# Kernel optimization log

Hardware: AMD Instinct MI355X
Metric: run time of the kernel (lower is better)

The kernel has to match this reference:

```python
import jax, jax.numpy as jnp
import numpy as np

QMIN, QMAX = -128, 127  # int8 range

def setup_inputs() -> dict:
    key = jax.random.key(0)
    k1, k2, k3 = jax.random.split(key, 3)
    B, S, DIN, DOUT = 8, 2048, 4096, 4096
    x = jax.random.normal(k1, (B, S, DIN), dtype=jnp.float32)
    weight = jax.random.normal(k2, (DOUT, DIN), dtype=jnp.float32) * 0.02
    bias = jax.random.normal(k3, (DOUT,), dtype=jnp.float32) * 0.01
    # per-tensor asymmetric activation qparams (as produced by a calibrated observer)
    act_scale = jnp.float32(0.05)
    act_zero_point = jnp.int32(3)
    # per-output-channel symmetric weight scales (block_size = (1, in_features))
    weight_scale = jnp.max(jnp.abs(weight), axis=1) / 127.0  # [DOUT]
    return {"x": x, "weight": weight, "bias": bias,
            "act_scale": act_scale, "act_zero_point": act_zero_point,
            "weight_scale": weight_scale}

def reference(x, weight, bias, act_scale, act_zero_point, weight_scale):
    # 1) quantize activations: per-tensor asymmetric int8
    qx = jnp.clip(jnp.round(x / act_scale) + act_zero_point, QMIN, QMAX).astype(jnp.int8)
    # 2) quantize weight: per-output-channel symmetric int8 (zero_point = 0)
    qw = jnp.clip(jnp.round(weight / weight_scale[:, None]), QMIN, QMAX).astype(jnp.int8)
    acc = jnp.einsum('bsk,nk->bsn',
                     qx.astype(jnp.int32) - act_zero_point.astype(jnp.int32),
                     qw.astype(jnp.int32))  # [B, S, DOUT] int32
    # 4) dequantize: combined scale = act_scale * weight_scale[n], then bias
    out = acc.astype(jnp.float32) * (act_scale * weight_scale) + bias
    return out
```

## Files before the change

### kernel.cpp

```cpp
#include <hip/hip_runtime.h>
#include <cstdint>

#define M_DIM 16384
#define N_DIM 4096
#define K_DIM 4096

#define BM 256
#define BN 256
#define BK 128

typedef __attribute__((ext_vector_type(4))) int int32x4;
typedef __attribute__((ext_vector_type(4))) float f32x4;

#define GLLD16(g, l)                                              \
  __builtin_amdgcn_global_load_lds(                               \
      (const __attribute__((address_space(1))) void*)(g),         \
      (__attribute__((address_space(3))) void*)(l), 16, 0, 0)

__global__ void quant_fused(const float* __restrict__ x,
                            const float* __restrict__ w,
                            const float* __restrict__ wscale,
                            const float* __restrict__ bias,
                            const float* __restrict__ sp,
                            const int* __restrict__ zpp,
                            int8_t* __restrict__ qx,
                            int8_t* __restrict__ qw,
                            float* __restrict__ cs,
                            float* __restrict__ off) {
  __shared__ int red[4];
  if (blockIdx.x < 16384) {
    const float rs = 1.0f / sp[0];
    const int zp = zpp[0];
    const size_t b = (size_t)blockIdx.x * 1024;
    const f32x4* x4 = (const f32x4*)x;
    unsigned* q4 = (unsigned*)qx;
#pragma unroll
    for (int i = 0; i < 4; i++) {
      const size_t idx = b + (size_t)i * 256 + threadIdx.x;
      f32x4 v = __builtin_nontemporal_load(&x4[idx]);
      int q0 = min(127, max(-128, (int)rintf(v[0] * rs) + zp));
      int q1 = min(127, max(-128, (int)rintf(v[1] * rs) + zp));
      int q2 = min(127, max(-128, (int)rintf(v[2] * rs) + zp));
      int q3 = min(127, max(-128, (int)rintf(v[3] * rs) + zp));
      q4[idx] = (unsigned)(q0 & 255) | ((unsigned)(q1 & 255) << 8) |
                ((unsigned)(q2 & 255) << 16) | ((unsigned)(q3 & 255) << 24);
    }
  } else {
    const int n = blockIdx.x - 16384;
    const float ws = wscale[n];
    const float rws = 1.0f / ws;
    const float s = sp[0];
    const int zp = zpp[0];
    const f32x4* wr = (const f32x4*)(w + (size_t)n * K_DIM);
    unsigned* qr = (unsigned*)(qw + (size_t)n * K_DIM);
    int sum = 0;
#pragma unroll
    for (int it = 0; it < K_DIM / (256 * 4); it++) {
      const int idx = it * 256 + threadIdx.x;
      f32x4 v = __builtin_nontemporal_load(&wr[idx]);
      int q0 = min(127, max(-128, (int)rintf(v[0] * rws)));
      int q1 = min(127, max(-128, (int)rintf(v[1] * rws)));
      int q2 = min(127, max(-128, (int)rintf(v[2] * rws)));
      int q3 = min(127, max(-128, (int)rintf(v[3] * rws)));
      sum += q0 + q1 + q2 + q3;
      qr[idx] = (unsigned)(q0 & 255) | ((unsigned)(q1 & 255) << 8) |
                ((unsigned)(q2 & 255) << 16) | ((unsigned)(q3 & 255) << 24);
    }
#pragma unroll
    for (int o = 32; o > 0; o >>= 1) sum += __shfl_down(sum, o, 64);
    if ((threadIdx.x & 63) == 0) red[threadIdx.x >> 6] = sum;
    __syncthreads();
    if (threadIdx.x == 0) {
      const int tot = red[0] + red[1] + red[2] + red[3];
      const float c = s * ws;
      cs[n] = c;
      off[n] = bias[n] - (float)(zp * tot) * c;
    }
  }
}

__global__ __launch_bounds__(512, 2) void gemm_i8(
    const int8_t* __restrict__ qx, const int8_t* __restrict__ qw,
    const float* __restrict__ cs, const float* __restrict__ off,
    float* __restrict__ out) {
  __shared__ __align__(16) int8_t lds[131072];

  const int tid = threadIdx.x;
  const int lane = tid & 63;
  const int wave = tid >> 6;
  const int wm = wave >> 2;
  const int wn = wave & 3;

  const int bid = blockIdx.x;
  const int swz = (bid & 7) * 128 + (bid >> 3);
  const int n0 = (swz & 15) * BN;
  const int m0 = (swz >> 4) * BM;

  int32x4 acc[8][4] = {};
  int32x4 af[8], bf0[4], bf1[4];

  const int scol = ((lane & 7) ^ ((lane >> 3) & 7)) * 16;
  const int8_t* pA[2][2];
  const int8_t* pB[2][2];
#pragma unroll
  for (int h = 0; h < 2; h++)
#pragma unroll
    for (int j = 0; j < 2; j++) {
      const int r = h * 128 + (wave * 2 + j) * 8 + (lane >> 3);
      const int ga = ((r >> 6) & 1) * 128 + (r >> 7) * 64 + (r & 63);
      const int gb = ((r >> 5) & 3) * 64 + (r >> 7) * 32 + (r & 31);
      pA[h][j] = qx + (size_t)(m0 + ga) * K_DIM + scol;
      pB[h][j] = qw + (size_t)(n0 + gb) * K_DIM + scol;
    }

  const int fr = lane & 15;
  const int quad = lane >> 4;
  int aoffs[8], boffs[4];
#pragma unroll
  for (int mtl = 0; mtl < 4; mtl++)
#pragma unroll
    for (int ks = 0; ks < 2; ks++) {
      const int r = wm * 64 + mtl * 16 + fr;
      const int c = (ks * 4 + quad) ^ (fr & 7);
      aoffs[mtl * 2 + ks] = r * 128 + c * 16;
    }
#pragma unroll
  for (int ntl = 0; ntl < 2; ntl++)
#pragma unroll
    for (int ks = 0; ks < 2; ks++) {
      const int r = wn * 32 + ntl * 16 + fr;
      const int c = (ks * 4 + quad) ^ (fr & 7);
      boffs[ntl * 2 + ks] = r * 128 + c * 16;
    }

#define STAGE(rbase, h, P, kb)                                          \
  do {                                                                  \
    GLLD16(P[h][0] + (kb), lds + (rbase) + (h) * 16384 + wave * 2048);  \
    GLLD16(P[h][1] + (kb),                                              \
           lds + (rbase) + (h) * 16384 + wave * 2048 + 1024);           \
  } while (0)

#define LDA(buf, h)                                                     \
  do {                                                                  \
    _Pragma("unroll") for (int q = 0; q < 8; q++) af[q] =               \
        *(const int32x4*)(lds + (buf) * 65536 + (h) * 16384 + aoffs[q]); \
  } while (0)

#define LDB(buf, g, BF)                                                 \
  do {                                                                  \
    _Pragma("unroll") for (int q = 0; q < 4; q++) BF[q] =               \
        *(const int32x4*)(lds + (buf) * 65536 + 32768 + (g) * 16384 +   \
                          boffs[q]);                                    \
  } while (0)

#define MM(h, g, BF)                                                       \
  do {                                                                    \
    _Pragma("unroll") for (int mtl = 0; mtl < 4; mtl++)                   \
        _Pragma("unroll") for (int ntl = 0; ntl < 2; ntl++) {             \
      acc[(h)*4 + mtl][(g)*2 + ntl] = __builtin_amdgcn_mfma_i32_16x16x64_i8( \
          BF[ntl * 2 + 0], af[mtl * 2 + 0], acc[(h)*4 + mtl][(g)*2 + ntl], \
          0, 0, 0);                                                        \
      acc[(h)*4 + mtl][(g)*2 + ntl] = __builtin_amdgcn_mfma_i32_16x16x64_i8( \
          BF[ntl * 2 + 1], af[mtl * 2 + 1], acc[(h)*4 + mtl][(g)*2 + ntl], \
          0, 0, 0);                                                        \
    }                                                                      \
  } while (0)

#define BAR() __builtin_amdgcn_s_barrier()
#define WAITLGKM() asm volatile("s_waitcnt lgkmcnt(0)" ::: "memory")
#define VM8() asm volatile("s_waitcnt vmcnt(8)" ::: "memory")
#define PRIO(x) __builtin_amdgcn_s_setprio(x)

  STAGE(0, 0, pA, 0);
  STAGE(0, 1, pA, 0);
  STAGE(32768, 0, pB, 0);
  STAGE(32768, 1, pB, 0);
  STAGE(65536, 0, pA, 128);
  STAGE(65536, 1, pA, 128);
  STAGE(98304, 0, pB, 128);
  STAGE(98304, 1, pB, 128);
  VM8();
  BAR();

  for (int i = 0; i < K_DIM / (2 * BK); i++) {
    const int kb1 = ((2 * i + 1) << 7) & (K_DIM - 1);
    const int kb2 = ((2 * i + 2) << 7) & (K_DIM - 1);
    const int kb3 = ((2 * i + 3) << 7) & (K_DIM - 1);
    LDA(0, 0);
    LDB(0, 0, bf0);
    LDB(0, 1, bf1);
    WAITLGKM();
    PRIO(1); MM(0, 0, bf0); PRIO(0);
    STAGE(65536, 1, pA, kb1);
    PRIO(1); MM(0, 1, bf1); PRIO(0);
    VM8();
    BAR();
    LDA(0, 1);
    WAITLGKM();
    PRIO(1); MM(1, 1, bf1); PRIO(0);
    STAGE(0, 0, pA, kb2);
    STAGE(32768, 0, pB, kb2);
    STAGE(32768, 1, pB, kb2);
    PRIO(1); MM(1, 0, bf0); PRIO(0);
    VM8();
    BAR();
    LDA(1, 0);
    LDB(1, 0, bf0);
    LDB(1, 1, bf1);
    WAITLGKM();
    PRIO(1); MM(0, 0, bf0); PRIO(0);
    STAGE(0, 1, pA, kb2);
    PRIO(1); MM(0, 1, bf1); PRIO(0);
    VM8();
    BAR();
    LDA(1, 1);
    WAITLGKM();
    PRIO(1); MM(1, 1, bf1); PRIO(0);
    STAGE(65536, 0, pA, kb3);
    STAGE(98304, 0, pB, kb3);
    STAGE(98304, 1, pB, kb3);
    PRIO(1); MM(1, 0, bf0); PRIO(0);
    VM8();
    BAR();
  }

#pragma unroll
  for (int nt = 0; nt < 4; nt++) {
    const int colb = n0 + wn * 64 + nt * 16 + quad * 4;
    const f32x4 c4 = *(const f32x4*)(cs + colb);
    const f32x4 o4 = *(const f32x4*)(off + colb);
#pragma unroll
    for (int mt = 0; mt < 8; mt++) {
      const int row = m0 + wm * 128 + mt * 16 + fr;
      f32x4 v;
      v[0] = (float)acc[mt][nt][0] * c4[0] + o4[0];
      v[1] = (float)acc[mt][nt][1] * c4[1] + o4[1];
      v[2] = (float)acc[mt][nt][2] * c4[2] + o4[2];
      v[3] = (float)acc[mt][nt][3] * c4[3] + o4[3];
      __builtin_nontemporal_store(
          v, (f32x4*)(out + (size_t)row * N_DIM + colb));
    }
  }
#undef STAGE
#undef LDA
#undef LDB
#undef MM
#undef BAR
#undef WAITLGKM
#undef VM8
#undef PRIO
}

extern "C" void kernel_launch(void* const* d_in, const int* in_sizes, int n_in,
                              void* d_out, int out_size, void* d_ws,
                              size_t ws_size, hipStream_t stream) {
  const float* x = (const float*)d_in[0];
  const float* w = (const float*)d_in[1];
  const float* bias = (const float*)d_in[2];
  const float* act_scale = (const float*)d_in[3];
  const int* zp = (const int*)d_in[4];
  const float* wscale = (const float*)d_in[5];
  float* out = (float*)d_out;

  int8_t* qx = (int8_t*)d_ws;
  int8_t* qw = qx + (size_t)M_DIM * K_DIM;
  float* cs = (float*)(qw + (size_t)N_DIM * K_DIM);
  float* off = cs + N_DIM;

  quant_fused<<<16384 + N_DIM, 256, 0, stream>>>(x, w, wscale, bias,
                                                 act_scale, zp, qx, qw, cs,
                                                 off);
  gemm_i8<<<dim3((M_DIM / BM) * (N_DIM / BN)), 512, 0, stream>>>(qx, qw, cs,
                                                                 off, out);
}
```

Measured before the change: 661.3 us.

## Double-buffer A fragments and prefetch LDS reads ahead of MFMA blocks

```diff
diff --git a/kernel.cpp b/kernel.cpp
--- a/kernel.cpp
+++ b/kernel.cpp
@@ -97,7 +97,7 @@
   const int m0 = (swz >> 4) * BM;
 
   int32x4 acc[8][4] = {};
-  int32x4 af[8], bf0[4], bf1[4];
+  int32x4 afA[8], afB[8], bf0[4], bf1[4];
 
   const int scol = ((lane & 7) ^ ((lane >> 3) & 7)) * 16;
   const int8_t* pA[2][2];
@@ -140,9 +140,9 @@
            lds + (rbase) + (h) * 16384 + wave * 2048 + 1024);           \
   } while (0)
 
-#define LDA(buf, h)                                                     \
+#define LDA(buf, h, AF)                                                 \
   do {                                                                  \
-    _Pragma("unroll") for (int q = 0; q < 8; q++) af[q] =               \
+    _Pragma("unroll") for (int q = 0; q < 8; q++) AF[q] =               \
         *(const int32x4*)(lds + (buf) * 65536 + (h) * 16384 + aoffs[q]); \
   } while (0)
 
@@ -153,22 +153,23 @@
                           boffs[q]);                                    \
   } while (0)
 
-#define MM(h, g, BF)                                                       \
+#define MM(h, g, BF, AF)                                                   \
   do {                                                                    \
     _Pragma("unroll") for (int mtl = 0; mtl < 4; mtl++)                   \
         _Pragma("unroll") for (int ntl = 0; ntl < 2; ntl++) {             \
       acc[(h)*4 + mtl][(g)*2 + ntl] = __builtin_amdgcn_mfma_i32_16x16x64_i8( \
-          BF[ntl * 2 + 0], af[mtl * 2 + 0], acc[(h)*4 + mtl][(g)*2 + ntl], \
+          BF[ntl * 2 + 0], AF[mtl * 2 + 0], acc[(h)*4 + mtl][(g)*2 + ntl], \
           0, 0, 0);                                                        \
       acc[(h)*4 + mtl][(g)*2 + ntl] = __builtin_amdgcn_mfma_i32_16x16x64_i8( \
-          BF[ntl * 2 + 1], af[mtl * 2 + 1], acc[(h)*4 + mtl][(g)*2 + ntl], \
+          BF[ntl * 2 + 1], AF[mtl * 2 + 1], acc[(h)*4 + mtl][(g)*2 + ntl], \
           0, 0, 0);                                                        \
     }                                                                      \
   } while (0)
 
 #define BAR() __builtin_amdgcn_s_barrier()
 #define WAITLGKM() asm volatile("s_waitcnt lgkmcnt(0)" ::: "memory")
-#define VM8() asm volatile("s_waitcnt vmcnt(8)" ::: "memory")
+#define VM2() asm volatile("s_waitcnt vmcnt(2)" ::: "memory")
+#define VM6() asm volatile("s_waitcnt vmcnt(6)" ::: "memory")
 #define PRIO(x) __builtin_amdgcn_s_setprio(x)
 
   STAGE(0, 0, pA, 0);
@@ -176,51 +177,53 @@
   STAGE(32768, 0, pB, 0);
   STAGE(32768, 1, pB, 0);
   STAGE(65536, 0, pA, 128);
-  STAGE(65536, 1, pA, 128);
   STAGE(98304, 0, pB, 128);
   STAGE(98304, 1, pB, 128);
-  VM8();
+  VM6();
   BAR();
+  LDA(0, 0, afA);
+  LDB(0, 0, bf0);
+  LDB(0, 1, bf1);
 
   for (int i = 0; i < K_DIM / (2 * BK); i++) {
     const int kb1 = ((2 * i + 1) << 7) & (K_DIM - 1);
     const int kb2 = ((2 * i + 2) << 7) & (K_DIM - 1);
     const int kb3 = ((2 * i + 3) << 7) & (K_DIM - 1);
-    LDA(0, 0);
-    LDB(0, 0, bf0);
-    LDB(0, 1, bf1);
-    WAITLGKM();
-    PRIO(1); MM(0, 0, bf0); PRIO(0);
+    WAITLGKM();
     STAGE(65536, 1, pA, kb1);
-    PRIO(1); MM(0, 1, bf1); PRIO(0);
-    VM8();
-    BAR();
-    LDA(0, 1);
-    WAITLGKM();
-    PRIO(1); MM(1, 1, bf1); PRIO(0);
+    LDA(0, 1, afB);
+    PRIO(1); MM(0, 0, bf0, afA); PRIO(0);
+    PRIO(1); MM(0, 1, bf1, afA); PRIO(0);
+    VM2();
+    BAR();
+    WAITLGKM();
     STAGE(0, 0, pA, kb2);
     STAGE(32768, 0, pB, kb2);
     STAGE(32768, 1, pB, kb2);
-    PRIO(1); MM(1, 0, bf0); PRIO(0);
-    VM8();
-    BAR();
-    LDA(1, 0);
+    LDA(1, 0, afA);
+    PRIO(1); MM(1, 1, bf1, afB); PRIO(0);
+    LDB(1, 1, bf1);
+    PRIO(1); MM(1, 0, bf0, afB); PRIO(0);
     LDB(1, 0, bf0);
-    LDB(1, 1, bf1);
-    WAITLGKM();
-    PRIO(1); MM(0, 0, bf0); PRIO(0);
+    VM6();
+    BAR();
+    WAITLGKM();
     STAGE(0, 1, pA, kb2);
-    PRIO(1); MM(0, 1, bf1); PRIO(0);
-    VM8();
-    BAR();
-    LDA(1, 1);
-    WAITLGKM();
-    PRIO(1); MM(1, 1, bf1); PRIO(0);
+    LDA(1, 1, afB);
+    PRIO(1); MM(0, 0, bf0, afA); PRIO(0);
+    PRIO(1); MM(0, 1, bf1, afA); PRIO(0);
+    VM2();
+    BAR();
+    WAITLGKM();
     STAGE(65536, 0, pA, kb3);
     STAGE(98304, 0, pB, kb3);
     STAGE(98304, 1, pB, kb3);
-    PRIO(1); MM(1, 0, bf0); PRIO(0);
-    VM8();
+    LDA(0, 0, afA);
+    PRIO(1); MM(1, 1, bf1, afB); PRIO(0);
+    LDB(0, 1, bf1);
+    PRIO(1); MM(1, 0, bf0, afB); PRIO(0);
+    LDB(0, 0, bf0);
+    VM6();
     BAR();
   }
 
@@ -247,7 +250,8 @@
 #undef MM
 #undef BAR
 #undef WAITLGKM
-#undef VM8
+#undef VM2
+#undef VM6
 #undef PRIO
 }
 
```

Result: slower. 741.9 us (+12.2%).
